# Performance work log

Hardware: AMD Instinct MI355X
Metric: run time of the kernel (lower is better)

Reference implementation:

```python
import jax, jax.numpy as jnp
import numpy as np

B, S, NT, D, NU = 1024, 200, 10000, 256, 100000
BETA_1 = 0.1


def setup_inputs() -> dict:
    key = jax.random.key(0)
    ks = jax.random.split(key, 6)
    user_id = jax.random.randint(ks[0], (B,), 0, NU)
    event_type = jax.random.randint(ks[1], (B, S), 0, NT + 1)  # 0 = pad
    adjacent_matrix = jax.random.uniform(ks[2], (NT, NT), dtype=jnp.float32)
    pop_encoding = jax.random.normal(ks[3], (NT + 1, D), dtype=jnp.float32)
    event_emb = jax.random.normal(ks[4], (NT + 1, D), dtype=jnp.float32) * 0.02
    user_emb = jax.random.normal(ks[5], (NU, D), dtype=jnp.float32) * 0.02
    return dict(user_id=user_id, event_type=event_type,
                adjacent_matrix=adjacent_matrix, pop_encoding=pop_encoding,
                evaluation=0, event_emb=event_emb, user_emb=user_emb)


def _l2norm(x, eps):
    # tf.nn.l2_normalize: x * rsqrt(max(sum(x^2), eps))
    return x * jax.lax.rsqrt(jnp.maximum(jnp.sum(x * x, axis=-1, keepdims=True), eps))


def reference(user_id, event_type, adjacent_matrix, pop_encoding, evaluation, event_emb, user_emb):
    non_pad = (event_type != 0).astype(jnp.float32)[..., None]          # [B,S,1]
    enc = event_emb[event_type]                                          # [B,S,D]
    usr = user_emb[user_id]                                              # [B,D]
    pop = pop_encoding[event_type] * non_pad                             # [B,S,D]
    # enc += sign(enc) * l2_normalize(user_output) (default eps 1e-12)
    enc = enc + jnp.sign(enc) * _l2norm(usr, 1e-12)[:, None, :]
    # per-sample adjacency: two-axis gather of the item-item matrix
    idx = jnp.where(event_type > 0, event_type - 1, 0)                   # [B,S]
    adj = adjacent_matrix[idx[:, :, None], idx[:, None, :]]              # [B,S,S]
    has_valid = (jnp.sum(event_type > 0, axis=1) > 0).astype(jnp.float32)
    adj = adj * has_valid[:, None, None]  # rows with all-pad stay zero, as in the loop
    output = jnp.mean(enc, axis=1)                                       # [B,D]
    user_embeddings = jnp.concatenate([output, jnp.mean(pop, axis=1) * BETA_1], axis=-1)  # [B,2D]
    if evaluation:
        item_encoding = event_emb[1:]                                    # [NT,D]
        scores = user_embeddings[:, :D] @ item_encoding.T
    else:
        item_encoding = jnp.concatenate([event_emb[1:], pop_encoding[1:] * BETA_1], axis=-1)  # [NT,2D]
        scores = user_embeddings @ item_encoding.T                       # [B,NT]
    prediction = jnp.tanh(_l2norm(scores, 1e-05))
    return prediction, user_embeddings, pop, adj
```

## Files before the change

kernel.cpp:

```cpp
#include <hip/hip_runtime.h>
#include <math.h>

#define NB 1024
#define NS 200
#define NTOK 10000
#define ND 256
#define BETA 0.1f

static constexpr size_t PRED_OFF = 0;
static constexpr size_t UE_OFF   = (size_t)NB * NTOK;
static constexpr size_t POP_OFF  = UE_OFF + (size_t)NB * 2 * ND;
static constexpr size_t ADJ_OFF  = POP_OFF + (size_t)NB * NS * ND;

static constexpr size_t WS_SIDX   = 0;
static constexpr size_t WS_HV     = WS_SIDX + (size_t)NB * NS;
static constexpr size_t WS_COUNTS = WS_HV + NB;
static constexpr size_t WS_OFFS   = WS_COUNTS + NTOK;
static constexpr size_t WS_CURSOR = WS_OFFS + NTOK + 1;
static constexpr size_t WS_PAIRS  = WS_CURSOR + NTOK;
static constexpr size_t WS_UEBF   = 440640;
static constexpr size_t WS_IEBF   = WS_UEBF + 262144;

typedef __attribute__((ext_vector_type(8))) short bf16x8;
typedef __attribute__((ext_vector_type(4))) float f32x4;
typedef __attribute__((ext_vector_type(8))) unsigned short u16x8;

static __device__ inline unsigned short f2bf(float f) {
    unsigned int u = __float_as_uint(f);
    return (unsigned short)((u + 0x7fffu + ((u >> 16) & 1u)) >> 16);
}

__global__ __launch_bounds__(256) void k_pre(
    const float* __restrict__ ee,
    const float* __restrict__ pe,
    unsigned short* __restrict__ ie,
    int* __restrict__ counts)
{
    const int blk = blockIdx.x;
    const int t = threadIdx.x;
    if (blk < 5000) {
        const int idx = blk * 256 + t;
        const int row = idx >> 7;
        const int kq  = idx & 127;
        float4 v; float sc;
        if (kq < 64) { v = *(const float4*)&ee[(size_t)(row + 1) * ND + kq * 4]; sc = 1.f; }
        else         { v = *(const float4*)&pe[(size_t)(row + 1) * ND + (kq - 64) * 4]; sc = BETA; }
        ushort4 h = {f2bf(v.x * sc), f2bf(v.y * sc), f2bf(v.z * sc), f2bf(v.w * sc)};
        *(ushort4*)&ie[(size_t)row * 512 + kq * 4] = h;
    } else {
        const int i = (blk - 5000) * 256 + t;
        if (i < NTOK) counts[i] = 0;
    }
}

__global__ __launch_bounds__(256) void k_embed(
    const int* __restrict__ user_id,
    const int* __restrict__ event_type,
    const float* __restrict__ pop_encoding,
    const float* __restrict__ event_emb,
    const float* __restrict__ user_emb,
    float* __restrict__ ue,
    unsigned short* __restrict__ ue_bf,
    float* __restrict__ pop,
    int* __restrict__ sidx_all,
    float* __restrict__ hvf,
    int* __restrict__ counts)
{
    const int b  = blockIdx.x;
    const int t  = threadIdx.x;
    const int sg = t >> 6;
    const int tl = t & 63;

    const int uid = user_id[b];
    const float4 u4 = *(const float4*)&user_emb[(size_t)uid * ND + tl * 4];

    float ss = u4.x * u4.x + u4.y * u4.y + u4.z * u4.z + u4.w * u4.w;
    #pragma unroll
    for (int o = 32; o > 0; o >>= 1) ss += __shfl_xor(ss, o, 64);
    const float rn = rsqrtf(fmaxf(ss, 1e-12f));
    const float4 nu4 = {u4.x * rn, u4.y * rn, u4.z * rn, u4.w * rn};

    __shared__ int et_s[NS];
    __shared__ int hv_s;
    if (t == 0) hv_s = 0;
    if (t < NS) et_s[t] = event_type[(size_t)b * NS + t];
    __syncthreads();

    if (t < NS) {
        const int et = et_s[t];
        const int r  = (et > 0) ? (et - 1) : 0;
        sidx_all[(size_t)b * NS + t] = r;
        atomicAdd(&counts[r], 1);
        if (et > 0) hv_s = 1;
    }

    float4 eacc = {0.f, 0.f, 0.f, 0.f};
    float4 pacc = {0.f, 0.f, 0.f, 0.f};
    #pragma unroll 2
    for (int it = 0; it < NS / 4; ++it) {
        const int s  = sg + 4 * it;
        const int et = et_s[s];
        const float4 e = *(const float4*)&event_emb[(size_t)et * ND + tl * 4];
        float4 p = *(const float4*)&pop_encoding[(size_t)et * ND + tl * 4];
        const float z = (et != 0) ? 1.f : 0.f;
        p.x *= z; p.y *= z; p.z *= z; p.w *= z;
        eacc.x += e.x + ((e.x > 0.f) ? nu4.x : ((e.x < 0.f) ? -nu4.x : 0.f));
        eacc.y += e.y + ((e.y > 0.f) ? nu4.y : ((e.y < 0.f) ? -nu4.y : 0.f));
        eacc.z += e.z + ((e.z > 0.f) ? nu4.z : ((e.z < 0.f) ? -nu4.z : 0.f));
        eacc.w += e.w + ((e.w > 0.f) ? nu4.w : ((e.w < 0.f) ? -nu4.w : 0.f));
        pacc.x += p.x; pacc.y += p.y; pacc.z += p.z; pacc.w += p.w;
        const f32x4 pv = {p.x, p.y, p.z, p.w};
        __builtin_nontemporal_store(pv, (f32x4*)&pop[((size_t)b * NS + s) * ND + tl * 4]);
    }

    __shared__ __align__(16) float4 es[4][64];
    __shared__ __align__(16) float4 ps[4][64];
    es[sg][tl] = eacc;
    ps[sg][tl] = pacc;
    __syncthreads();

    if (t < 128) {
        const int half = t >> 6;
        const int l2   = t & 63;
        float4 f = half ? ps[0][l2] : es[0][l2];
        #pragma unroll
        for (int w = 1; w < 4; ++w) {
            const float4 g = half ? ps[w][l2] : es[w][l2];
            f.x += g.x; f.y += g.y; f.z += g.z; f.w += g.w;
        }
        const float sc = half ? (BETA / NS) : (1.f / NS);
        const float4 o = {f.x * sc, f.y * sc, f.z * sc, f.w * sc};
        const size_t off = (size_t)b * 512 + half * 256 + l2 * 4;
        *(float4*)&ue[off] = o;
        ushort4 h = {f2bf(o.x), f2bf(o.y), f2bf(o.z), f2bf(o.w)};
        *(ushort4*)&ue_bf[off] = h;
    }
    if (t == 0) hvf[b] = hv_s ? 1.f : 0.f;
}

#define SCAN_CHUNK 40
__global__ __launch_bounds__(256) void k_scan(
    const int* __restrict__ counts,
    int* __restrict__ offsets,
    int* __restrict__ cursor)
{
    const int t = threadIdx.x;
    int sum = 0;
    int local[SCAN_CHUNK];
    #pragma unroll
    for (int k = 0; k < SCAN_CHUNK; ++k) {
        const int idx = t * SCAN_CHUNK + k;
        const int c = (idx < NTOK) ? counts[idx] : 0;
        local[k] = c;
        sum += c;
    }
    __shared__ int part[256];
    part[t] = sum;
    __syncthreads();
    for (int o = 1; o < 256; o <<= 1) {
        const int v = (t >= o) ? part[t - o] : 0;
        __syncthreads();
        part[t] += v;
        __syncthreads();
    }
    int running = part[t] - sum;
    #pragma unroll
    for (int k = 0; k < SCAN_CHUNK; ++k) {
        const int idx = t * SCAN_CHUNK + k;
        if (idx < NTOK) {
            offsets[idx] = running;
            cursor[idx]  = running;
            running += local[k];
        }
    }
    if (t == 255) offsets[NTOK] = part[255];
}

__global__ __launch_bounds__(256) void k_scatter(
    const int* __restrict__ sidx_all,
    int* __restrict__ cursor,
    int* __restrict__ pairs)
{
    const int b = blockIdx.x;
    const int t = threadIdx.x;
    if (t < NS) {
        const int r = sidx_all[(size_t)b * NS + t];
        const int slot = atomicAdd(&cursor[r], 1);
        pairs[slot] = b * NS + t;
    }
}

__global__ __launch_bounds__(512) void k_adj2(
    const float* __restrict__ A,
    const int* __restrict__ sidx_all,
    const int* __restrict__ offsets,
    const int* __restrict__ pairs,
    const float* __restrict__ hvf,
    float* __restrict__ adj)
{
    const int r = blockIdx.x;
    const int t = threadIdx.x;
    const int p0 = offsets[r];
    const int n  = offsets[r + 1] - p0;
    if (n == 0) return;

    __shared__ __align__(16) float rowlds[NTOK];
    const float4* Arow = (const float4*)(A + (size_t)r * NTOK);
    #pragma unroll 5
    for (int l = t; l < NTOK / 4; l += 512)
        ((float4*)rowlds)[l] = Arow[l];
    __syncthreads();

    const int wave = t >> 6, lane = t & 63;
    #pragma unroll 2
    for (int pi = wave; pi < n; pi += 8) {
        const int pv = pairs[p0 + pi];
        const int b  = pv / NS;
        const float hv = hvf[b];
        if (lane < 50) {
            const int4 c4 = *(const int4*)&sidx_all[(size_t)b * NS + lane * 4];
            f32x4 v;
            v.x = rowlds[c4.x] * hv;
            v.y = rowlds[c4.y] * hv;
            v.z = rowlds[c4.z] * hv;
            v.w = rowlds[c4.w] * hv;
            __builtin_nontemporal_store(v, (f32x4*)&adj[(size_t)pv * NS + lane * 4]);
        }
    }
}

#define GBM 128
#define GBN 128
#define GBK 32
#define LDK 40

__global__ __launch_bounds__(256) void k_gemm_mfma(
    const unsigned short* __restrict__ ue_bf,
    const unsigned short* __restrict__ ie_bf,
    float* __restrict__ scores)
{
    __shared__ __align__(16) unsigned short As[GBM * LDK];
    __shared__ __align__(16) unsigned short Bs[GBN * LDK];

    const int t  = threadIdx.x;
    const int bn = blockIdx.x, bm = blockIdx.y;
    const int m0 = bm * GBM, n0 = bn * GBN;

    const int wave = t >> 6, lane = t & 63;
    const int ww = wave & 1, wm = wave >> 1;
    const int lr = lane & 15;
    const int kg = lane >> 4;

    f32x4 acc[4][4] = {};

    for (int k0 = 0; k0 < 512; k0 += GBK) {
        #pragma unroll
        for (int i = 0; i < 2; ++i) {
            const int c = t + 256 * i;
            const int row = c >> 2, q = c & 3;
            *(u16x8*)&As[row * LDK + q * 8] =
                *(const u16x8*)&ue_bf[(size_t)(m0 + row) * 512 + k0 + q * 8];
        }
        #pragma unroll
        for (int i = 0; i < 2; ++i) {
            const int c = t + 256 * i;
            const int row = c >> 2, q = c & 3;
            const int gn = n0 + row;
            u16x8 h = {0, 0, 0, 0, 0, 0, 0, 0};
            if (gn < NTOK)
                h = *(const u16x8*)&ie_bf[(size_t)gn * 512 + k0 + q * 8];
            *(u16x8*)&Bs[row * LDK + q * 8] = h;
        }
        __syncthreads();

        bf16x8 a[4], b[4];
        #pragma unroll
        for (int mf = 0; mf < 4; ++mf)
            a[mf] = *(const bf16x8*)&As[(wm * 64 + mf * 16 + lr) * LDK + kg * 8];
        #pragma unroll
        for (int nf = 0; nf < 4; ++nf)
            b[nf] = *(const bf16x8*)&Bs[(ww * 64 + nf * 16 + lr) * LDK + kg * 8];
        #pragma unroll
        for (int mf = 0; mf < 4; ++mf)
            #pragma unroll
            for (int nf = 0; nf < 4; ++nf)
                acc[mf][nf] = __builtin_amdgcn_mfma_f32_16x16x32_bf16(
                    a[mf], b[nf], acc[mf][nf], 0, 0, 0);
        __syncthreads();
    }

    #pragma unroll
    for (int mf = 0; mf < 4; ++mf) {
        const int row = m0 + wm * 64 + mf * 16 + kg * 4;
        #pragma unroll
        for (int nf = 0; nf < 4; ++nf) {
            const int col = n0 + ww * 64 + nf * 16 + lr;
            if (col < NTOK) {
                #pragma unroll
                for (int r = 0; r < 4; ++r)
                    scores[(size_t)(row + r) * NTOK + col] = acc[mf][nf][r];
            }
        }
    }
}

__global__ __launch_bounds__(256) void k_norm(float* __restrict__ scores)
{
    const int b = blockIdx.x;
    const int t = threadIdx.x;
    float4* row4 = (float4*)(scores + (size_t)b * NTOK);

    float ss = 0.f;
    for (int l = t; l < NTOK / 4; l += 256) {
        const float4 v = row4[l];
        ss += v.x * v.x + v.y * v.y + v.z * v.z + v.w * v.w;
    }
    #pragma unroll
    for (int o = 32; o > 0; o >>= 1) ss += __shfl_down(ss, o, 64);
    __shared__ float wss[4];
    const int wid = t >> 6, lane = t & 63;
    if (lane == 0) wss[wid] = ss;
    __syncthreads();
    const float tot = wss[0] + wss[1] + wss[2] + wss[3];
    const float rs = rsqrtf(fmaxf(tot, 1e-5f));

    for (int l = t; l < NTOK / 4; l += 256) {
        float4 v = row4[l];
        v.x = tanhf(v.x * rs); v.y = tanhf(v.y * rs);
        v.z = tanhf(v.z * rs); v.w = tanhf(v.w * rs);
        row4[l] = v;
    }
}

extern "C" void kernel_launch(void* const* d_in, const int* in_sizes, int n_in,
                              void* d_out, int out_size, void* d_ws, size_t ws_size,
                              hipStream_t stream) {
    const int*   user_id      = (const int*)d_in[0];
    const int*   event_type   = (const int*)d_in[1];
    const float* adjacent     = (const float*)d_in[2];
    const float* pop_encoding = (const float*)d_in[3];
    const float* event_emb    = (const float*)d_in[5];
    const float* user_emb     = (const float*)d_in[6];

    float* out  = (float*)d_out;
    float* pred = out + PRED_OFF;
    float* ue   = out + UE_OFF;
    float* pop  = out + POP_OFF;
    float* adj  = out + ADJ_OFF;

    int*   ws       = (int*)d_ws;
    int*   sidx_all = ws + WS_SIDX;
    float* hvf      = (float*)(ws + WS_HV);
    int*   counts   = ws + WS_COUNTS;
    int*   offsets  = ws + WS_OFFS;
    int*   cursor   = ws + WS_CURSOR;
    int*   pairs    = ws + WS_PAIRS;
    unsigned short* ue_bf = (unsigned short*)(ws + WS_UEBF);
    unsigned short* ie_bf = (unsigned short*)(ws + WS_IEBF);

    k_pre<<<5000 + (NTOK + 255) / 256, 256, 0, stream>>>(event_emb, pop_encoding,
                                                         ie_bf, counts);
    k_embed<<<NB, 256, 0, stream>>>(user_id, event_type, pop_encoding,
                                    event_emb, user_emb, ue, ue_bf, pop,
                                    sidx_all, hvf, counts);
    k_scan<<<1, 256, 0, stream>>>(counts, offsets, cursor);
    k_scatter<<<NB, 256, 0, stream>>>(sidx_all, cursor, pairs);
    k_adj2<<<NTOK, 512, 0, stream>>>(adjacent, sidx_all, offsets, pairs, hvf, adj);

    dim3 ggrid((NTOK + GBN - 1) / GBN, NB / GBM);
    k_gemm_mfma<<<ggrid, 256, 0, stream>>>(ue_bf, ie_bf, pred);
    k_norm<<<NB, 256, 0, stream>>>(pred);
}
```

Measured before the change: 316.2 us.

## Merge pre/embed and GEMM/adjacency kernels, histogram counts in shared memory

Folds the bf16 item-encoding conversion into the embedding kernel as extra blocks. The adjacency gather and the MFMA GEMM now run as block ranges of a single launch, so they can overlap on the GPU. The per-token histogram moves from global atomics in the embed kernel to shared-memory atomics inside the single-block scan kernel. This removes two launches and the global atomic contention. In exchange, the single-block scan must now read all 204,800 indices serially, and the adjacency blocks drop from 512 to 256 threads.

```diff
diff --git a/kernel.cpp b/kernel.cpp
--- a/kernel.cpp
+++ b/kernel.cpp
@@ -30,30 +30,7 @@
     return (unsigned short)((u + 0x7fffu + ((u >> 16) & 1u)) >> 16);
 }
 
-__global__ __launch_bounds__(256) void k_pre(
-    const float* __restrict__ ee,
-    const float* __restrict__ pe,
-    unsigned short* __restrict__ ie,
-    int* __restrict__ counts)
-{
-    const int blk = blockIdx.x;
-    const int t = threadIdx.x;
-    if (blk < 5000) {
-        const int idx = blk * 256 + t;
-        const int row = idx >> 7;
-        const int kq  = idx & 127;
-        float4 v; float sc;
-        if (kq < 64) { v = *(const float4*)&ee[(size_t)(row + 1) * ND + kq * 4]; sc = 1.f; }
-        else         { v = *(const float4*)&pe[(size_t)(row + 1) * ND + (kq - 64) * 4]; sc = BETA; }
-        ushort4 h = {f2bf(v.x * sc), f2bf(v.y * sc), f2bf(v.z * sc), f2bf(v.w * sc)};
-        *(ushort4*)&ie[(size_t)row * 512 + kq * 4] = h;
-    } else {
-        const int i = (blk - 5000) * 256 + t;
-        if (i < NTOK) counts[i] = 0;
-    }
-}
-
-__global__ __launch_bounds__(256) void k_embed(
+__global__ __launch_bounds__(256) void k_front(
     const int* __restrict__ user_id,
     const int* __restrict__ event_type,
     const float* __restrict__ pop_encoding,
@@ -64,10 +41,23 @@
     float* __restrict__ pop,
     int* __restrict__ sidx_all,
     float* __restrict__ hvf,
-    int* __restrict__ counts)
-{
+    unsigned short* __restrict__ ie)
+{
+    const int t = threadIdx.x;
+
+    if (blockIdx.x >= NB) {
+        const int idx = (blockIdx.x - NB) * 256 + t;
+        const int row = idx >> 7;
+        const int kq  = idx & 127;
+        float4 v; float sc;
+        if (kq < 64) { v = *(const float4*)&event_emb[(size_t)(row + 1) * ND + kq * 4]; sc = 1.f; }
+        else         { v = *(const float4*)&pop_encoding[(size_t)(row + 1) * ND + (kq - 64) * 4]; sc = BETA; }
+        ushort4 h = {f2bf(v.x * sc), f2bf(v.y * sc), f2bf(v.z * sc), f2bf(v.w * sc)};
+        *(ushort4*)&ie[(size_t)row * 512 + kq * 4] = h;
+        return;
+    }
+
     const int b  = blockIdx.x;
-    const int t  = threadIdx.x;
     const int sg = t >> 6;
     const int tl = t & 63;
 
@@ -88,9 +78,7 @@
 
     if (t < NS) {
         const int et = et_s[t];
-        const int r  = (et > 0) ? (et - 1) : 0;
-        sidx_all[(size_t)b * NS + t] = r;
-        atomicAdd(&counts[r], 1);
+        sidx_all[(size_t)b * NS + t] = (et > 0) ? (et - 1) : 0;
         if (et > 0) hv_s = 1;
     }
 
@@ -140,17 +128,31 @@
 
 #define SCAN_CHUNK 40
 __global__ __launch_bounds__(256) void k_scan(
-    const int* __restrict__ counts,
+    const int* __restrict__ sidx_all,
     int* __restrict__ offsets,
     int* __restrict__ cursor)
 {
     const int t = threadIdx.x;
+    __shared__ int cnt[NTOK];
+    for (int i = t; i < NTOK; i += 256) cnt[i] = 0;
+    __syncthreads();
+
+    const int4* s4 = (const int4*)sidx_all;
+    for (int i = t; i < NB * NS / 4; i += 256) {
+        const int4 v = s4[i];
+        atomicAdd(&cnt[v.x], 1);
+        atomicAdd(&cnt[v.y], 1);
+        atomicAdd(&cnt[v.z], 1);
+        atomicAdd(&cnt[v.w], 1);
+    }
+    __syncthreads();
+
     int sum = 0;
     int local[SCAN_CHUNK];
     #pragma unroll
     for (int k = 0; k < SCAN_CHUNK; ++k) {
         const int idx = t * SCAN_CHUNK + k;
-        const int c = (idx < NTOK) ? counts[idx] : 0;
+        const int c = (idx < NTOK) ? cnt[idx] : 0;
         local[k] = c;
         sum += c;
     }
@@ -190,7 +192,16 @@
     }
 }
 
-__global__ __launch_bounds__(512) void k_adj2(
+#define GBM 128
+#define GBN 128
+#define GBK 32
+#define LDK 40
+#define NGEMM 632
+
+__global__ __launch_bounds__(256) void k_main(
+    const unsigned short* __restrict__ ue_bf,
+    const unsigned short* __restrict__ ie_bf,
+    float* __restrict__ scores,
     const float* __restrict__ A,
     const int* __restrict__ sidx_all,
     const int* __restrict__ offsets,
@@ -198,22 +209,90 @@
     const float* __restrict__ hvf,
     float* __restrict__ adj)
 {
-    const int r = blockIdx.x;
-    const int t = threadIdx.x;
+    __shared__ __align__(16) unsigned char smem[40960];
+    const int t = threadIdx.x;
+
+    if (blockIdx.x < NGEMM) {
+        unsigned short* As = (unsigned short*)smem;
+        unsigned short* Bs = As + GBM * LDK;
+
+        const int g  = blockIdx.x;
+        const int bn = g % 79, bm = g / 79;
+        const int m0 = bm * GBM, n0 = bn * GBN;
+
+        const int wave = t >> 6, lane = t & 63;
+        const int ww = wave & 1, wm = wave >> 1;
+        const int lr = lane & 15;
+        const int kg = lane >> 4;
+
+        f32x4 acc[4][4] = {};
+
+        for (int k0 = 0; k0 < 512; k0 += GBK) {
+            #pragma unroll
+            for (int i = 0; i < 2; ++i) {
+                const int c = t + 256 * i;
+                const int row = c >> 2, q = c & 3;
+                *(u16x8*)&As[row * LDK + q * 8] =
+                    *(const u16x8*)&ue_bf[(size_t)(m0 + row) * 512 + k0 + q * 8];
+            }
+            #pragma unroll
+            for (int i = 0; i < 2; ++i) {
+                const int c = t + 256 * i;
+                const int row = c >> 2, q = c & 3;
+                const int gn = n0 + row;
+                u16x8 h = {0, 0, 0, 0, 0, 0, 0, 0};
+                if (gn < NTOK)
+                    h = *(const u16x8*)&ie_bf[(size_t)gn * 512 + k0 + q * 8];
+                *(u16x8*)&Bs[row * LDK + q * 8] = h;
+            }
+            __syncthreads();
+
+            bf16x8 a[4], b[4];
+            #pragma unroll
+            for (int mf = 0; mf < 4; ++mf)
+                a[mf] = *(const bf16x8*)&As[(wm * 64 + mf * 16 + lr) * LDK + kg * 8];
+            #pragma unroll
+            for (int nf = 0; nf < 4; ++nf)
+                b[nf] = *(const bf16x8*)&Bs[(ww * 64 + nf * 16 + lr) * LDK + kg * 8];
+            #pragma unroll
+            for (int mf = 0; mf < 4; ++mf)
+                #pragma unroll
+                for (int nf = 0; nf < 4; ++nf)
+                    acc[mf][nf] = __builtin_amdgcn_mfma_f32_16x16x32_bf16(
+                        a[mf], b[nf], acc[mf][nf], 0, 0, 0);
+            __syncthreads();
+        }
+
+        #pragma unroll
+        for (int mf = 0; mf < 4; ++mf) {
+            const int row = m0 + wm * 64 + mf * 16 + kg * 4;
+            #pragma unroll
+            for (int nf = 0; nf < 4; ++nf) {
+                const int col = n0 + ww * 64 + nf * 16 + lr;
+                if (col < NTOK) {
+                    #pragma unroll
+                    for (int r = 0; r < 4; ++r)
+                        scores[(size_t)(row + r) * NTOK + col] = acc[mf][nf][r];
+                }
+            }
+        }
+        return;
+    }
+
+    const int r = blockIdx.x - NGEMM;
     const int p0 = offsets[r];
     const int n  = offsets[r + 1] - p0;
     if (n == 0) return;
 
-    __shared__ __align__(16) float rowlds[NTOK];
+    float* rowlds = (float*)smem;
     const float4* Arow = (const float4*)(A + (size_t)r * NTOK);
-    #pragma unroll 5
-    for (int l = t; l < NTOK / 4; l += 512)
+    #pragma unroll 4
+    for (int l = t; l < NTOK / 4; l += 256)
         ((float4*)rowlds)[l] = Arow[l];
     __syncthreads();
 
     const int wave = t >> 6, lane = t & 63;
-    #pragma unroll 2
-    for (int pi = wave; pi < n; pi += 8) {
+    for (int pi = wave; pi < n; pi += 4) {
         const int pv = pairs[p0 + pi];
         const int b  = pv / NS;
         const float hv = hvf[b];
@@ -229,81 +308,6 @@
     }
 }
 
-#define GBM 128
-#define GBN 128
-#define GBK 32
-#define LDK 40
-
-__global__ __launch_bounds__(256) void k_gemm_mfma(
-    const unsigned short* __restrict__ ue_bf,
-    const unsigned short* __restrict__ ie_bf,
-    float* __restrict__ scores)
-{
-    __shared__ __align__(16) unsigned short As[GBM * LDK];
-    __shared__ __align__(16) unsigned short Bs[GBN * LDK];
-
-    const int t  = threadIdx.x;
-    const int bn = blockIdx.x, bm = blockIdx.y;
-    const int m0 = bm * GBM, n0 = bn * GBN;
-
-    const int wave = t >> 6, lane = t & 63;
-    const int ww = wave & 1, wm = wave >> 1;
-    const int lr = lane & 15;
-    const int kg = lane >> 4;
-
-    f32x4 acc[4][4] = {};
-
-    for (int k0 = 0; k0 < 512; k0 += GBK) {
-        #pragma unroll
-        for (int i = 0; i < 2; ++i) {
-            const int c = t + 256 * i;
-            const int row = c >> 2, q = c & 3;
-            *(u16x8*)&As[row * LDK + q * 8] =
-                *(const u16x8*)&ue_bf[(size_t)(m0 + row) * 512 + k0 + q * 8];
-        }
-        #pragma unroll
-        for (int i = 0; i < 2; ++i) {
-            const int c = t + 256 * i;
-            const int row = c >> 2, q = c & 3;
-            const int gn = n0 + row;
-            u16x8 h = {0, 0, 0, 0, 0, 0, 0, 0};
-            if (gn < NTOK)
-                h = *(const u16x8*)&ie_bf[(size_t)gn * 512 + k0 + q * 8];
-            *(u16x8*)&Bs[row * LDK + q * 8] = h;
-        }
-        __syncthreads();
-
-        bf16x8 a[4], b[4];
-        #pragma unroll
-        for (int mf = 0; mf < 4; ++mf)
-            a[mf] = *(const bf16x8*)&As[(wm * 64 + mf * 16 + lr) * LDK + kg * 8];
-        #pragma unroll
-        for (int nf = 0; nf < 4; ++nf)
-            b[nf] = *(const bf16x8*)&Bs[(ww * 64 + nf * 16 + lr) * LDK + kg * 8];
-        #pragma unroll
-        for (int mf = 0; mf < 4; ++mf)
-            #pragma unroll
-            for (int nf = 0; nf < 4; ++nf)
-                acc[mf][nf] = __builtin_amdgcn_mfma_f32_16x16x32_bf16(
-                    a[mf], b[nf], acc[mf][nf], 0, 0, 0);
-        __syncthreads();
-    }
-
-    #pragma unroll
-    for (int mf = 0; mf < 4; ++mf) {
-        const int row = m0 + wm * 64 + mf * 16 + kg * 4;
-        #pragma unroll
-        for (int nf = 0; nf < 4; ++nf) {
-            const int col = n0 + ww * 64 + nf * 16 + lr;
-            if (col < NTOK) {
-                #pragma unroll
-                for (int r = 0; r < 4; ++r)
-                    scores[(size_t)(row + r) * NTOK + col] = acc[mf][nf][r];
-            }
-        }
-    }
-}
-
 __global__ __launch_bounds__(256) void k_norm(float* __restrict__ scores)
 {
     const int b = blockIdx.x;
@@ -351,23 +355,19 @@
     int*   ws       = (int*)d_ws;
     int*   sidx_all = ws + WS_SIDX;
     float* hvf      = (float*)(ws + WS_HV);
-    int*   counts   = ws + WS_COUNTS;
     int*   offsets  = ws + WS_OFFS;
     int*   cursor   = ws + WS_CURSOR;
     int*   pairs    = ws + WS_PAIRS;
     unsigned short* ue_bf = (unsigned short*)(ws + WS_UEBF);
     unsigned short* ie_bf = (unsigned short*)(ws + WS_IEBF);
 
-    k_pre<<<5000 + (NTOK + 255) / 256, 256, 0, stream>>>(event_emb, pop_encoding,
-                                                         ie_bf, counts);
-    k_embed<<<NB, 256, 0, stream>>>(user_id, event_type, pop_encoding,
-                                    event_emb, user_emb, ue, ue_bf, pop,
-                                    sidx_all, hvf, counts);
-    k_scan<<<1, 256, 0, stream>>>(counts, offsets, cursor);
+    k_front<<<NB + 5000, 256, 0, stream>>>(user_id, event_type, pop_encoding,
+                                           event_emb, user_emb, ue, ue_bf, pop,
+                                           sidx_all, hvf, ie_bf);
+    k_scan<<<1, 256, 0, stream>>>(sidx_all, offsets, cursor);
     k_scatter<<<NB, 256, 0, stream>>>(sidx_all, cursor, pairs);
-    k_adj2<<<NTOK, 512, 0, stream>>>(adjacent, sidx_all, offsets, pairs, hvf, adj);
-
-    dim3 ggrid((NTOK + GBN - 1) / GBN, NB / GBM);
-    k_gemm_mfma<<<ggrid, 256, 0, stream>>>(ue_bf, ie_bf, pred);
+    k_main<<<NGEMM + NTOK, 256, 0, stream>>>(ue_bf, ie_bf, pred,
+                                             adjacent, sidx_all, offsets, pairs,
+                                             hvf, adj);
     k_norm<<<NB, 256, 0, stream>>>(pred);
 }
```

Result: slower. 370.6 us (+17.2%).
